# Kernel tuning notes

Measured on AMD Instinct MI355X. Metric: run time of the kernel, lower is better.

## Reference

```python
import jax, jax.numpy as jnp
import numpy as np

N_ATOMS = 200000
N_EDGES = 6400000
N_TYPES = 4
COULOMB = 14.399645478425668  # e^2 / (4 pi eps0) in eV*Angstrom
P_EXP = 0.23
A0 = 0.4685


def _phi(r, c, da):
    # r: (E,), c: (4,), da: (4, E) -> (E,)
    return jnp.sum(c[:, None] * jnp.exp(-r * da), axis=0)


def _dphi(r, c, da):
    return jnp.sum(-c[:, None] * da * jnp.exp(-r * da), axis=0)


def _d2phi(r, c, da):
    return jnp.sum(c[:, None] * da ** 2 * jnp.exp(-r * da), axis=0)


def setup_inputs() -> dict:
    key = jax.random.key(0)
    k1, k2, k3, k4 = jax.random.split(key, 4)
    rij = jax.random.uniform(k1, (N_EDGES,), dtype=jnp.float32) * 2.0 + 0.1
    first_atom = jax.random.randint(k2, (N_EDGES,), 0, N_ATOMS, dtype=jnp.int32)
    second_atom = jax.random.randint(k3, (N_EDGES,), 0, N_ATOMS, dtype=jnp.int32)
    atom_type_index = jax.random.randint(k4, (N_ATOMS,), 0, N_TYPES, dtype=jnp.int32)
    # ASE covalent radii for H, C, N, O (Angstrom) and atomic numbers
    covalent_radii = jnp.array([0.31, 0.76, 0.71, 0.66], dtype=jnp.float32)
    atomic_numbers = jnp.array([1.0, 6.0, 7.0, 8.0], dtype=jnp.float32)
    return {
        "rij": rij,
        "covalent_radii": covalent_radii,
        "atomic_numbers": atomic_numbers,
        "first_atom": first_atom,
        "second_atom": second_atom,
        "atom_type_index": atom_type_index,
        "n_atoms": N_ATOMS,
    }


def reference(rij, covalent_radii, atomic_numbers, first_atom, second_atom, atom_type_index, n_atoms):
    # ZBL 4-term exponential screening coefficients
    c = jnp.array([0.02817, 0.28022, 0.50986, 0.18175], dtype=rij.dtype)
    d = jnp.array([0.20162, 0.4029, 0.94229, 3.1998], dtype=rij.dtype)

    ti = atom_type_index[first_atom]   # (E,)
    tj = atom_type_index[second_atom]  # (E,)
    zi = atomic_numbers[ti]
    zj = atomic_numbers[tj]
    rc = covalent_radii[ti] + covalent_radii[tj]  # outer cutoff per pair

    a = A0 / (zi ** P_EXP + zj ** P_EXP)  # (E,)
    da = d[:, None] / a                    # (4, E)
    factor = COULOMB * zi * zj             # (E,)

    # energy at rij
    e = factor / rij * _phi(rij, c, da)

    # switching polynomial matched at rc (r1 = 0)
    phi_c = _phi(rc, c, da)
    dphi_c = _dphi(rc, c, da)
    d2phi_c = _d2phi(rc, c, da)
    ec = factor / rc * phi_c
    dec = factor / rc * (-phi_c / rc + dphi_c)
    d2ec = factor / rc * (d2phi_c - 2.0 / rc * dphi_c + 2.0 * phi_c / rc ** 2)

    A = (-3.0 * dec + rc * d2ec) / rc ** 2
    B = (2.0 * dec - rc * d2ec) / rc ** 3
    C = -ec + rc * dec / 2.0 - rc * rc * d2ec / 12.0

    e = e + A / 3.0 * rij ** 3 + B / 4.0 * rij ** 4 + C
    e = e / 2.0
    e = jnp.where(rij > rc, jnp.zeros_like(e), e)

    # scatter pair energies onto first atom of each pair
    e_nodes = jax.ops.segment_sum(e, first_atom, num_segments=n_atoms)
    return e_nodes
```

## Files before the change

kernel.cpp:

```cpp
#include <hip/hip_runtime.h>


#define TPB_PACK  256
#define P1_BLOCKS 512
#define P1_TPB    1024
#define SB_BITS   14
#define SBS       (1 << SB_BITS)
#define NS_FUSE   13
#define NS_MAX    16
#define P2_TPB    1024
#define R_SUB     39
#define TPB_RED   256
#define CAP_MAX   1024

#define TAB_N   258
#define TAB_L0  (-3.3219281f)
#define TAB_HL  (0.017157490f)
#define TAB_INV (58.283567f)
#define TAB_OFF (193.61423f)

__global__ __launch_bounds__(P1_TPB) void zbl_bin3(
    const float* __restrict__ rij,
    const float* __restrict__ rcov,
    const float* __restrict__ znum,
    const int*  __restrict__ fa,
    const int*  __restrict__ sa,
    const int*  __restrict__ types,
    unsigned int* __restrict__ regions,
    int*   __restrict__ counts,
    uint2* __restrict__ ovf,
    int E, int nquad, int natoms, int nwords, int NS, int cap, int chunkQ,
    int ovfStride)
{
    __shared__ unsigned s_pk[NS_FUSE * SBS / 16];
    __shared__ float  tabE[16 * TAB_N];
    __shared__ float4 cB[16];
    __shared__ float4 cS[16];
    __shared__ float  cC[16];
    __shared__ int    scnt[NS_MAX];
    __shared__ int    s_ovfn;

    const int b   = blockIdx.x;
    const int tid = threadIdx.x;

    if (tid < NS)  scnt[tid] = 0;
    if (tid == 32) s_ovfn = 0;

    {
        const int4* t4 = (const int4*)types;
        for (int w = tid; w < nwords; w += P1_TPB) {
            unsigned word = 0;
            if (((w << 4) + 16) <= natoms) {
                int b4 = w << 2;
                #pragma unroll
                for (int g = 0; g < 4; ++g) {
                    int4 v = t4[b4 + g];
                    word |= ((unsigned)v.x & 3u) << (8 * g + 0);
                    word |= ((unsigned)v.y & 3u) << (8 * g + 2);
                    word |= ((unsigned)v.z & 3u) << (8 * g + 4);
                    word |= ((unsigned)v.w & 3u) << (8 * g + 6);
                }
            } else {
                int base = w << 4;
                for (int j = 0; j < 16; ++j) {
                    int i = base + j;
                    unsigned t = (i < natoms) ? (unsigned)types[i] : 0u;
                    word |= (t & 3u) << (2 * j);
                }
            }
            s_pk[w] = word;
        }
    }

    if (tid < 16) {
        const float cc[4] = {0.02817f, 0.28022f, 0.50986f, 0.18175f};
        const float dd[4] = {0.20162f, 0.4029f, 0.94229f, 3.1998f};
        const float COUL = 14.399645478425668f;
        int t = tid;
        int ti = t >> 2, tj = t & 3;
        float zi = znum[ti], zj = znum[tj];
        float rc = rcov[ti] + rcov[tj];
        float a = 0.4685f / (powf(zi, 0.23f) + powf(zj, 0.23f));
        float inva = 1.0f / a;
        float factor = COUL * zi * zj;
        float da[4], ee[4];
        float phi = 0.0f, dphi = 0.0f, d2phi = 0.0f;
        #pragma unroll
        for (int k = 0; k < 4; ++k) {
            da[k] = dd[k] * inva;
            ee[k] = expf(-rc * da[k]);
            phi   += cc[k] * ee[k];
            dphi  -= cc[k] * da[k] * ee[k];
            d2phi += cc[k] * da[k] * da[k] * ee[k];
        }
        float invrc = 1.0f / rc;
        float ec   = factor * invrc * phi;
        float dec  = factor * invrc * (-phi * invrc + dphi);
        float d2ec = factor * invrc * (d2phi - 2.0f * invrc * dphi + 2.0f * phi * invrc * invrc);
        float A = (-3.0f * dec + rc * d2ec) * invrc * invrc;
        float B = (2.0f * dec - rc * d2ec) * invrc * invrc * invrc;
        float Cc = -ec + 0.5f * rc * dec - rc * rc * d2ec * (1.0f / 12.0f);
        const float L2E = 1.4426950408889634f;
        cB[t] = make_float4(rc, 0.5f * factor, A * (1.0f / 6.0f), B * 0.125f);
        cS[t] = make_float4(-da[0] * L2E, -da[1] * L2E, -da[2] * L2E, -da[3] * L2E);
        cC[t] = Cc * 0.5f;
    }
    __syncthreads();

    const float lc0 = -5.1497481f;
    const float lc1 = -1.8353434f;
    const float lc2 = -0.9718340f;
    const float lc3 = -2.4600449f;

    for (int n = tid; n < 16 * TAB_N; n += P1_TPB) {
        int t = n / TAB_N, k = n - t * TAB_N;
        float v = 0.0f;
        if (k <= 256) {
            float r = exp2f(__builtin_fmaf((float)k, TAB_HL, TAB_L0));
            float4 B = cB[t];
            if (r <= B.x) {
                float4 S = cS[t];
                float p = exp2f(__builtin_fmaf(r, S.x, lc0))
                        + exp2f(__builtin_fmaf(r, S.y, lc1))
                        + exp2f(__builtin_fmaf(r, S.z, lc2))
                        + exp2f(__builtin_fmaf(r, S.w, lc3));
                float r3 = r * r * r;
                float poly = __builtin_fmaf(__builtin_fmaf(B.w, r, B.z), r3, cC[t]);
                v = __builtin_fmaf(B.y * p, 1.0f / r, poly);
            }
        }
        tabE[n] = v;
    }
    __syncthreads();

    const float4* rij4 = (const float4*)rij;
    const int4*   fa4  = (const int4*)fa;
    const int4*   sa4  = (const int4*)sa;
    int myreg = b * NS;
    int q0 = b * chunkQ;
    int q1 = q0 + chunkQ; if (q1 > nquad) q1 = nquad;

    for (int q = q0 + tid; q < q1; q += P1_TPB) {
        float4 rv = rij4[q];
        int4   iv = fa4[q];
        int4   jv = sa4[q];
        float ra[4] = {rv.x, rv.y, rv.z, rv.w};
        int   ia[4] = {iv.x, iv.y, iv.z, iv.w};
        int   ja[4] = {jv.x, jv.y, jv.z, jv.w};
        float eo[4];
        #pragma unroll
        for (int k = 0; k < 4; ++k) {
            int i = ia[k], j = ja[k];
            unsigned wi = s_pk[i >> 4], wj = s_pk[j >> 4];
            unsigned ti = (wi >> ((i & 15) * 2)) & 3u;
            unsigned tj = (wj >> ((j & 15) * 2)) & 3u;
            int t = (int)((ti << 2) | tj);
            float kf = __builtin_fmaf(__log2f(ra[k]), TAB_INV, TAB_OFF);
            int ki = (int)kf;
            ki = ki < 0 ? 0 : (ki > 256 ? 256 : ki);
            float frac = kf - (float)ki;
            int base = t * TAB_N + ki;
            float v0 = tabE[base];
            float v1 = tabE[base + 1];
            eo[k] = __builtin_fmaf(v1 - v0, frac, v0);
        }
        #pragma unroll
        for (int k = 0; k < 4; ++k) {
            if (eo[k] != 0.0f) {
                int atom = ia[k];
                int s = atom >> SB_BITS;
                int slot = atomicAdd(&scnt[s], 1);
                if (slot < cap) {
                    unsigned rec = ((__float_as_uint(eo[k]) + 0x2000u) & 0xFFFFC000u)
                                 | (unsigned)(atom & (SBS - 1));
                    regions[(unsigned)((myreg + s) * cap + slot)] = rec;
                } else {
                    int o = atomicAdd(&s_ovfn, 1);
                    ovf[(size_t)b * ovfStride + o] =
                        make_uint2(__float_as_uint(eo[k]), (unsigned)atom);
                }
            }
        }
    }

    if (b == 0) {
        for (int idx = nquad * 4 + tid; idx < E; idx += P1_TPB) {
            int i = fa[idx], j = sa[idx];
            unsigned wi = s_pk[i >> 4], wj = s_pk[j >> 4];
            int t = (int)((((wi >> ((i & 15) * 2)) & 3u) << 2) |
                           ((wj >> ((j & 15) * 2)) & 3u));
            float r = rij[idx];
            float kf = __builtin_fmaf(__log2f(r), TAB_INV, TAB_OFF);
            int ki = (int)kf;
            ki = ki < 0 ? 0 : (ki > 256 ? 256 : ki);
            float frac = kf - (float)ki;
            int base = t * TAB_N + ki;
            float e = __builtin_fmaf(tabE[base + 1] - tabE[base], frac, tabE[base]);
            if (e != 0.0f) {
                int o = atomicAdd(&s_ovfn, 1);
                ovf[(size_t)b * ovfStride + o] =
                    make_uint2(__float_as_uint(e), (unsigned)i);
            }
        }
    }

    __syncthreads();
    if (tid < NS)  counts[tid * P1_BLOCKS + b] = min(scnt[tid], cap);
    if (tid == NS) counts[NS  * P1_BLOCKS + b] = s_ovfn;
}

__global__ __launch_bounds__(P2_TPB) void zbl_agg(
    const unsigned int* __restrict__ regions,
    const int*  __restrict__ counts,
    float* __restrict__ partials,
    int NS, int cap)
{
    __shared__ float acc[SBS];
    int s = blockIdx.x, r = blockIdx.y;
    float4* acc4 = (float4*)acc;
    for (int i = threadIdx.x; i < SBS / 4; i += P2_TPB)
        acc4[i] = make_float4(0.f, 0.f, 0.f, 0.f);
    __syncthreads();
    int wave = threadIdx.x >> 6, lane = threadIdx.x & 63;
    const int NW = P2_TPB >> 6;
    for (int p = r + wave * R_SUB; p < P1_BLOCKS; p += NW * R_SUB) {
        int n = counts[s * P1_BLOCKS + p];
        size_t base = ((size_t)p * NS + s) * (size_t)cap;
        for (int t = lane; t < n; t += 64) {
            unsigned rec = regions[base + t];
            atomicAdd(&acc[rec & (SBS - 1)],
                      __uint_as_float(rec & 0xFFFFC000u));
        }
    }
    __syncthreads();
    float4* dst4 = (float4*)(partials + ((size_t)s * R_SUB + r) * SBS);
    for (int i = threadIdx.x; i < SBS / 4; i += P2_TPB)
        dst4[i] = acc4[i];
}

__global__ __launch_bounds__(TPB_RED) void zbl_red3(
    const float* __restrict__ partials,
    const int*   __restrict__ counts,
    const uint2* __restrict__ ovf,
    float* __restrict__ out,
    int natoms, int NS, int ovfStride)
{
    __shared__ int s_any;
    int tid = threadIdx.x;
    int q = blockIdx.x * TPB_RED + tid;
    int nq = natoms >> 2;

    float4 acc = make_float4(0.f, 0.f, 0.f, 0.f);
    int atom0 = q << 2;
    if (q < nq) {
        int s = atom0 >> SB_BITS, i = atom0 & (SBS - 1);
        const float* p = partials + (size_t)s * R_SUB * SBS + i;
        #pragma unroll
        for (int k = 0; k < R_SUB; ++k) {
            float4 v = *(const float4*)(p + (size_t)k * SBS);
            acc.x += v.x; acc.y += v.y; acc.z += v.z; acc.w += v.w;
        }
    }

    if (tid == 0) s_any = 0;
    __syncthreads();
    for (int p0 = tid; p0 < P1_BLOCKS; p0 += TPB_RED) {
        int n = counts[NS * P1_BLOCKS + p0];
        if (n > 0) atomicAdd(&s_any, n);
    }
    __syncthreads();
    if (s_any > 0 && q < nq) {
        for (int p = 0; p < P1_BLOCKS; ++p) {
            int n = counts[NS * P1_BLOCKS + p];
            const uint2* lst = ovf + (size_t)p * ovfStride;
            for (int e = 0; e < n; ++e) {
                uint2 rec = lst[e];
                int d = (int)rec.y - atom0;
                if ((unsigned)d < 4u) {
                    float v = __uint_as_float(rec.x);
                    if      (d == 0) acc.x += v;
                    else if (d == 1) acc.y += v;
                    else if (d == 2) acc.z += v;
                    else             acc.w += v;
                }
            }
        }
    }
    if (q < nq) *(float4*)(out + atom0) = acc;

    if (blockIdx.x == 0 && tid < (natoms & 3)) {
        int atom = (nq << 2) + tid;
        int s = atom >> SB_BITS, i = atom & (SBS - 1);
        const float* p = partials + (size_t)s * R_SUB * SBS + i;
        float a = 0.f;
        #pragma unroll
        for (int k = 0; k < R_SUB; ++k) a += p[(size_t)k * SBS];
        if (s_any > 0) {
            for (int pp = 0; pp < P1_BLOCKS; ++pp) {
                int n = counts[NS * P1_BLOCKS + pp];
                const uint2* lst = ovf + (size_t)pp * ovfStride;
                for (int e = 0; e < n; ++e)
                    if ((int)lst[e].y == atom) a += __uint_as_float(lst[e].x);
            }
        }
        out[atom] = a;
    }
}

__global__ __launch_bounds__(TPB_PACK) void zbl_pack(
    const int* __restrict__ types, unsigned int* __restrict__ packed,
    float* __restrict__ fallback, int natoms, int nwords)
{
    int tid = blockIdx.x * TPB_PACK + threadIdx.x;
    int nth = gridDim.x * TPB_PACK;
    for (int w = tid; w < nwords; w += nth) {
        int base = w << 4;
        unsigned int word = 0;
        #pragma unroll
        for (int j = 0; j < 16; ++j) {
            int i = base + j;
            unsigned int t = (i < natoms) ? (unsigned int)types[i] : 0u;
            word |= (t & 3u) << (2 * j);
        }
        packed[w] = word;
    }
    for (int i = tid; i < natoms; i += nth) fallback[i] = 0.0f;
}

__global__ __launch_bounds__(P1_TPB) void zbl_bin(
    const float* __restrict__ rij, const float* __restrict__ rcov,
    const float* __restrict__ znum, const int* __restrict__ fa,
    const int* __restrict__ sa, const unsigned int* __restrict__ packed,
    unsigned int* __restrict__ regions, int* __restrict__ counts,
    float* __restrict__ fallback,
    int E, int nquad, int natoms, int nwords, int NS, int cap, int chunkQ)
{
    extern __shared__ unsigned int s_packed[];
    __shared__ float  tabE[16 * TAB_N];
    __shared__ float4 cB[16];
    __shared__ float4 cS[16];
    __shared__ float  cC[16];
    __shared__ int scnt[NS_MAX];

    for (int w = threadIdx.x; w < nwords; w += P1_TPB) s_packed[w] = packed[w];
    if (threadIdx.x < NS) scnt[threadIdx.x] = 0;

    if (threadIdx.x < 16) {
        const float cc[4] = {0.02817f, 0.28022f, 0.50986f, 0.18175f};
        const float dd[4] = {0.20162f, 0.4029f, 0.94229f, 3.1998f};
        const float COUL = 14.399645478425668f;
        int t = threadIdx.x;
        int ti = t >> 2, tj = t & 3;
        float zi = znum[ti], zj = znum[tj];
        float rc = rcov[ti] + rcov[tj];
        float a = 0.4685f / (powf(zi, 0.23f) + powf(zj, 0.23f));
        float inva = 1.0f / a;
        float factor = COUL * zi * zj;
        float da[4], ee[4];
        float phi = 0.0f, dphi = 0.0f, d2phi = 0.0f;
        #pragma unroll
        for (int k = 0; k < 4; ++k) {
            da[k] = dd[k] * inva;
            ee[k] = expf(-rc * da[k]);
            phi   += cc[k] * ee[k];
            dphi  -= cc[k] * da[k] * ee[k];
            d2phi += cc[k] * da[k] * da[k] * ee[k];
        }
        float invrc = 1.0f / rc;
        float ec   = factor * invrc * phi;
        float dec  = factor * invrc * (-phi * invrc + dphi);
        float d2ec = factor * invrc * (d2phi - 2.0f * invrc * dphi + 2.0f * phi * invrc * invrc);
        float A = (-3.0f * dec + rc * d2ec) * invrc * invrc;
        float B = (2.0f * dec - rc * d2ec) * invrc * invrc * invrc;
        float Cc = -ec + 0.5f * rc * dec - rc * rc * d2ec * (1.0f / 12.0f);
        const float L2E = 1.4426950408889634f;
        cB[t] = make_float4(rc, 0.5f * factor, A * (1.0f / 6.0f), B * 0.125f);
        cS[t] = make_float4(-da[0] * L2E, -da[1] * L2E, -da[2] * L2E, -da[3] * L2E);
        cC[t] = Cc * 0.5f;
    }
    __syncthreads();

    const float lc0 = -5.1497481f, lc1 = -1.8353434f;
    const float lc2 = -0.9718340f, lc3 = -2.4600449f;

    for (int n = threadIdx.x; n < 16 * TAB_N; n += P1_TPB) {
        int t = n / TAB_N, k = n - t * TAB_N;
        float v = 0.0f;
        if (k <= 256) {
            float r = exp2f(__builtin_fmaf((float)k, TAB_HL, TAB_L0));
            float4 B = cB[t];
            if (r <= B.x) {
                float4 S = cS[t];
                float p = exp2f(__builtin_fmaf(r, S.x, lc0))
                        + exp2f(__builtin_fmaf(r, S.y, lc1))
                        + exp2f(__builtin_fmaf(r, S.z, lc2))
                        + exp2f(__builtin_fmaf(r, S.w, lc3));
                float r3 = r * r * r;
                float poly = __builtin_fmaf(__builtin_fmaf(B.w, r, B.z), r3, cC[t]);
                v = __builtin_fmaf(B.y * p, 1.0f / r, poly);
            }
        }
        tabE[n] = v;
    }
    __syncthreads();

    const float4* rij4 = (const float4*)rij;
    const int4*   fa4  = (const int4*)fa;
    const int4*   sa4  = (const int4*)sa;
    int myreg = blockIdx.x * NS;
    int q0 = blockIdx.x * chunkQ;
    int q1 = q0 + chunkQ; if (q1 > nquad) q1 = nquad;

    for (int q = q0 + threadIdx.x; q < q1; q += P1_TPB) {
        float4 rv = rij4[q];
        int4   iv = fa4[q];
        int4   jv = sa4[q];
        float ra[4] = {rv.x, rv.y, rv.z, rv.w};
        int   ia[4] = {iv.x, iv.y, iv.z, iv.w};
        int   ja[4] = {jv.x, jv.y, jv.z, jv.w};
        float eo[4];
        #pragma unroll
        for (int k = 0; k < 4; ++k) {
            int i = ia[k], j = ja[k];
            unsigned int wi = s_packed[i >> 4], wj = s_packed[j >> 4];
            unsigned int ti = (wi >> ((i & 15) * 2)) & 3u;
            unsigned int tj = (wj >> ((j & 15) * 2)) & 3u;
            int t = (int)((ti << 2) | tj);
            float kf = __builtin_fmaf(__log2f(ra[k]), TAB_INV, TAB_OFF);
            int ki = (int)kf;
            ki = ki < 0 ? 0 : (ki > 256 ? 256 : ki);
            float frac = kf - (float)ki;
            int base = t * TAB_N + ki;
            float v0 = tabE[base], v1 = tabE[base + 1];
            eo[k] = __builtin_fmaf(v1 - v0, frac, v0);
        }
        #pragma unroll
        for (int k = 0; k < 4; ++k) {
            if (eo[k] != 0.0f) {
                int atom = ia[k];
                int s = atom >> SB_BITS;
                int slot = atomicAdd(&scnt[s], 1);
                if (slot < cap) {
                    unsigned rec = ((__float_as_uint(eo[k]) + 0x2000u) & 0xFFFFC000u)
                                 | (unsigned)(atom & (SBS - 1));
                    regions[(unsigned)((myreg + s) * cap + slot)] = rec;
                } else {
                    unsafeAtomicAdd(&fallback[atom], eo[k]);
                }
            }
        }
    }

    if (blockIdx.x == 0) {
        for (int idx = nquad * 4 + threadIdx.x; idx < E; idx += P1_TPB) {
            int i = fa[idx], j = sa[idx];
            unsigned int wi = s_packed[i >> 4], wj = s_packed[j >> 4];
            int t = (int)((((wi >> ((i & 15) * 2)) & 3u) << 2) |
                           ((wj >> ((j & 15) * 2)) & 3u));
            float r = rij[idx];
            float kf = __builtin_fmaf(__log2f(r), TAB_INV, TAB_OFF);
            int ki = (int)kf;
            ki = ki < 0 ? 0 : (ki > 256 ? 256 : ki);
            float frac = kf - (float)ki;
            int base = t * TAB_N + ki;
            float e = __builtin_fmaf(tabE[base + 1] - tabE[base], frac, tabE[base]);
            if (e != 0.0f) unsafeAtomicAdd(&fallback[i], e);
        }
    }

    __syncthreads();
    if (cap > 0 && threadIdx.x < NS)
        counts[threadIdx.x * P1_BLOCKS + blockIdx.x] = min(scnt[threadIdx.x], cap);
}

__global__ __launch_bounds__(TPB_RED) void zbl_red(
    const float* __restrict__ partials, const float* __restrict__ fallback,
    float* __restrict__ out, int natoms)
{
    int q = blockIdx.x * TPB_RED + threadIdx.x;
    int nq = natoms >> 2;
    if (q < nq) {
        int atom = q << 2;
        int s = atom >> SB_BITS, i = atom & (SBS - 1);
        const float4* fb4 = (const float4*)(fallback + atom);
        float4 acc = *fb4;
        const float* p = partials + (size_t)s * R_SUB * SBS + i;
        #pragma unroll
        for (int k = 0; k < R_SUB; ++k) {
            float4 v = *(const float4*)(p + (size_t)k * SBS);
            acc.x += v.x; acc.y += v.y; acc.z += v.z; acc.w += v.w;
        }
        *(float4*)(out + atom) = acc;
    }
    if (blockIdx.x == 0 && threadIdx.x < (natoms & 3)) {
        int atom = (nq << 2) + threadIdx.x;
        int s = atom >> SB_BITS, i = atom & (SBS - 1);
        float acc = fallback[atom];
        const float* p = partials + (size_t)s * R_SUB * SBS + i;
        #pragma unroll
        for (int k = 0; k < R_SUB; ++k) acc += p[(size_t)k * SBS];
        out[atom] = acc;
    }
}

static inline size_t al256(size_t x) { return (x + 255) & ~(size_t)255; }

extern "C" void kernel_launch(void* const* d_in, const int* in_sizes, int n_in,
                              void* d_out, int out_size, void* d_ws, size_t ws_size,
                              hipStream_t stream) {
    const float* rij  = (const float*)d_in[0];
    const float* rcov = (const float*)d_in[1];
    const float* znum = (const float*)d_in[2];
    const int*   fa   = (const int*)d_in[3];
    const int*   sa   = (const int*)d_in[4];
    const int*   types= (const int*)d_in[5];
    float* out = (float*)d_out;
    int E = in_sizes[0];
    int natoms = out_size;
    int nquad = E / 4;
    int nwords = (natoms + 15) / 16;
    int NS = (natoms + SBS - 1) >> SB_BITS;
    if (NS > NS_MAX) NS = NS_MAX;
    int chunkQ = (nquad + P1_BLOCKS - 1) / P1_BLOCKS;
    int ovfStride = chunkQ * 4 + 8;

    if (natoms <= NS_FUSE * SBS) {
        size_t cnt_b  = al256((size_t)(NS + 1) * P1_BLOCKS * 4);
        size_t ovf_b  = al256((size_t)P1_BLOCKS * ovfStride * 8);
        size_t part_b = al256((size_t)NS * R_SUB * SBS * 4);
        char* base = (char*)d_ws;
        int*   counts   = (int*)base;                        base += cnt_b;
        uint2* ovf      = (uint2*)base;                      base += ovf_b;
        float* partials = (float*)base;                      base += part_b;
        unsigned int* regions = (unsigned int*)base;

        long long avail = (long long)ws_size - (long long)(cnt_b + ovf_b + part_b);
        int cap = 0;
        if (avail > 0) cap = (int)(avail / ((long long)P1_BLOCKS * NS * 4));
        if (cap > CAP_MAX) cap = CAP_MAX;

        if (cap >= 64) {
            zbl_bin3<<<P1_BLOCKS, P1_TPB, 0, stream>>>(
                rij, rcov, znum, fa, sa, types,
                regions, counts, ovf,
                E, nquad, natoms, nwords, NS, cap, chunkQ, ovfStride);
            dim3 g2(NS, R_SUB);
            zbl_agg<<<g2, P2_TPB, 0, stream>>>(regions, counts, partials, NS, cap);
            int nq = natoms >> 2;
            zbl_red3<<<(nq + TPB_RED - 1) / TPB_RED, TPB_RED, 0, stream>>>(
                partials, counts, ovf, out, natoms, NS, ovfStride);
            return;
        }
    }

    size_t packed_bytes = al256((size_t)nwords * 4);
    size_t cnt_bytes    = al256((size_t)NS * P1_BLOCKS * 4);
    size_t fb_bytes     = al256((size_t)natoms * 4);
    size_t part_bytes   = al256((size_t)NS * R_SUB * SBS * 4);
    unsigned int* packed = (unsigned int*)d_ws;
    int*   counts   = (int*)  ((char*)d_ws + packed_bytes);
    float* fallback = (float*)((char*)d_ws + packed_bytes + cnt_bytes);
    float* partials = (float*)((char*)d_ws + packed_bytes + cnt_bytes + fb_bytes);
    unsigned int* regions = (unsigned int*)((char*)d_ws + packed_bytes + cnt_bytes
                                            + fb_bytes + part_bytes);
    long long avail = (long long)ws_size
                    - (long long)(packed_bytes + cnt_bytes + fb_bytes + part_bytes);
    int cap = 0;
    if (avail > 0) cap = (int)(avail / ((long long)P1_BLOCKS * (long long)NS * 4));
    if (cap > CAP_MAX) cap = CAP_MAX;
    size_t smem = (size_t)nwords * sizeof(unsigned int);

    if (cap >= 64) {
        zbl_pack<<<96, TPB_PACK, 0, stream>>>(types, packed, fallback, natoms, nwords);
        zbl_bin<<<P1_BLOCKS, P1_TPB, smem, stream>>>(
            rij, rcov, znum, fa, sa, packed, regions, counts, fallback,
            E, nquad, natoms, nwords, NS, cap, chunkQ);
        dim3 g2(NS, R_SUB);
        zbl_agg<<<g2, P2_TPB, 0, stream>>>(regions, counts, partials, NS, cap);
        int nq = natoms >> 2;
        zbl_red<<<(nq + TPB_RED - 1) / TPB_RED, TPB_RED, 0, stream>>>(
            partials, fallback, out, natoms);
    } else {
        zbl_pack<<<96, TPB_PACK, 0, stream>>>(types, packed, out, natoms, nwords);
        zbl_bin<<<P1_BLOCKS, P1_TPB, smem, stream>>>(
            rij, rcov, znum, fa, sa, packed, regions, counts, out,
            E, nquad, natoms, nwords, NS, 0, chunkQ);
    }
}
```

Before: 175.0 us.

## Fuse bin, aggregate and reduce stages into one cooperative kernel

```diff
diff --git a/kernel.cpp b/kernel.cpp
--- a/kernel.cpp
+++ b/kernel.cpp
@@ -1,5 +1,8 @@
 #include <hip/hip_runtime.h>
-
+#include <hip/hip_cooperative_groups.h>
+
+
+namespace cg = cooperative_groups;
 
 #define TPB_PACK  256
 #define P1_BLOCKS 512
@@ -19,58 +22,65 @@
 #define TAB_INV (58.283567f)
 #define TAB_OFF (193.61423f)
 
-__global__ __launch_bounds__(P1_TPB) void zbl_bin3(
+__global__ __launch_bounds__(P1_TPB, 8) void zbl_coop(
     const float* __restrict__ rij,
     const float* __restrict__ rcov,
     const float* __restrict__ znum,
     const int*  __restrict__ fa,
     const int*  __restrict__ sa,
     const int*  __restrict__ types,
+    unsigned int* __restrict__ packed,
     unsigned int* __restrict__ regions,
     int*   __restrict__ counts,
     uint2* __restrict__ ovf,
+    float* __restrict__ partials,
+    float* __restrict__ out,
     int E, int nquad, int natoms, int nwords, int NS, int cap, int chunkQ,
     int ovfStride)
 {
-    __shared__ unsigned s_pk[NS_FUSE * SBS / 16];
-    __shared__ float  tabE[16 * TAB_N];
+    cg::grid_group grid = cg::this_grid();
+
+    __shared__ union {
+        struct { unsigned pk[NS_FUSE * SBS / 16]; float tabE[16 * TAB_N]; } a;
+        float  acc[SBS];
+        float4 acc4[SBS / 4];
+    } u;
     __shared__ float4 cB[16];
     __shared__ float4 cS[16];
     __shared__ float  cC[16];
     __shared__ int    scnt[NS_MAX];
     __shared__ int    s_ovfn;
+    __shared__ int    s_any;
 
     const int b   = blockIdx.x;
     const int tid = threadIdx.x;
 
+    for (int w = b + P1_BLOCKS * tid; w < nwords; w += P1_BLOCKS * P1_TPB) {
+        unsigned word = 0;
+        if (((w << 4) + 16) <= natoms) {
+            const int4* t4 = (const int4*)types;
+            int b4 = w << 2;
+            #pragma unroll
+            for (int g = 0; g < 4; ++g) {
+                int4 v = t4[b4 + g];
+                word |= ((unsigned)v.x & 3u) << (8 * g + 0);
+                word |= ((unsigned)v.y & 3u) << (8 * g + 2);
+                word |= ((unsigned)v.z & 3u) << (8 * g + 4);
+                word |= ((unsigned)v.w & 3u) << (8 * g + 6);
+            }
+        } else {
+            int base = w << 4;
+            for (int j = 0; j < 16; ++j) {
+                int i = base + j;
+                unsigned t = (i < natoms) ? (unsigned)types[i] : 0u;
+                word |= (t & 3u) << (2 * j);
+            }
+        }
+        packed[w] = word;
+    }
+
     if (tid < NS)  scnt[tid] = 0;
     if (tid == 32) s_ovfn = 0;
-
-    {
-        const int4* t4 = (const int4*)types;
-        for (int w = tid; w < nwords; w += P1_TPB) {
-            unsigned word = 0;
-            if (((w << 4) + 16) <= natoms) {
-                int b4 = w << 2;
-                #pragma unroll
-                for (int g = 0; g < 4; ++g) {
-                    int4 v = t4[b4 + g];
-                    word |= ((unsigned)v.x & 3u) << (8 * g + 0);
-                    word |= ((unsigned)v.y & 3u) << (8 * g + 2);
-                    word |= ((unsigned)v.z & 3u) << (8 * g + 4);
-                    word |= ((unsigned)v.w & 3u) << (8 * g + 6);
-                }
-            } else {
-                int base = w << 4;
-                for (int j = 0; j < 16; ++j) {
-                    int i = base + j;
-                    unsigned t = (i < natoms) ? (unsigned)types[i] : 0u;
-                    word |= (t & 3u) << (2 * j);
-                }
-            }
-            s_pk[w] = word;
-        }
-    }
 
     if (tid < 16) {
         const float cc[4] = {0.02817f, 0.28022f, 0.50986f, 0.18175f};
@@ -107,203 +117,209 @@
     }
     __syncthreads();
 
-    const float lc0 = -5.1497481f;
-    const float lc1 = -1.8353434f;
-    const float lc2 = -0.9718340f;
-    const float lc3 = -2.4600449f;
-
-    for (int n = tid; n < 16 * TAB_N; n += P1_TPB) {
-        int t = n / TAB_N, k = n - t * TAB_N;
-        float v = 0.0f;
-        if (k <= 256) {
-            float r = exp2f(__builtin_fmaf((float)k, TAB_HL, TAB_L0));
-            float4 B = cB[t];
-            if (r <= B.x) {
-                float4 S = cS[t];
-                float p = exp2f(__builtin_fmaf(r, S.x, lc0))
-                        + exp2f(__builtin_fmaf(r, S.y, lc1))
-                        + exp2f(__builtin_fmaf(r, S.z, lc2))
-                        + exp2f(__builtin_fmaf(r, S.w, lc3));
-                float r3 = r * r * r;
-                float poly = __builtin_fmaf(__builtin_fmaf(B.w, r, B.z), r3, cC[t]);
-                v = __builtin_fmaf(B.y * p, 1.0f / r, poly);
-            }
-        }
-        tabE[n] = v;
-    }
-    __syncthreads();
-
-    const float4* rij4 = (const float4*)rij;
-    const int4*   fa4  = (const int4*)fa;
-    const int4*   sa4  = (const int4*)sa;
-    int myreg = b * NS;
-    int q0 = b * chunkQ;
-    int q1 = q0 + chunkQ; if (q1 > nquad) q1 = nquad;
-
-    for (int q = q0 + tid; q < q1; q += P1_TPB) {
-        float4 rv = rij4[q];
-        int4   iv = fa4[q];
-        int4   jv = sa4[q];
-        float ra[4] = {rv.x, rv.y, rv.z, rv.w};
-        int   ia[4] = {iv.x, iv.y, iv.z, iv.w};
-        int   ja[4] = {jv.x, jv.y, jv.z, jv.w};
-        float eo[4];
-        #pragma unroll
-        for (int k = 0; k < 4; ++k) {
-            int i = ia[k], j = ja[k];
-            unsigned wi = s_pk[i >> 4], wj = s_pk[j >> 4];
-            unsigned ti = (wi >> ((i & 15) * 2)) & 3u;
-            unsigned tj = (wj >> ((j & 15) * 2)) & 3u;
-            int t = (int)((ti << 2) | tj);
-            float kf = __builtin_fmaf(__log2f(ra[k]), TAB_INV, TAB_OFF);
-            int ki = (int)kf;
-            ki = ki < 0 ? 0 : (ki > 256 ? 256 : ki);
-            float frac = kf - (float)ki;
-            int base = t * TAB_N + ki;
-            float v0 = tabE[base];
-            float v1 = tabE[base + 1];
-            eo[k] = __builtin_fmaf(v1 - v0, frac, v0);
-        }
-        #pragma unroll
-        for (int k = 0; k < 4; ++k) {
-            if (eo[k] != 0.0f) {
-                int atom = ia[k];
-                int s = atom >> SB_BITS;
-                int slot = atomicAdd(&scnt[s], 1);
-                if (slot < cap) {
-                    unsigned rec = ((__float_as_uint(eo[k]) + 0x2000u) & 0xFFFFC000u)
-                                 | (unsigned)(atom & (SBS - 1));
-                    regions[(unsigned)((myreg + s) * cap + slot)] = rec;
-                } else {
+    {
+        const float lc0 = -5.1497481f;
+        const float lc1 = -1.8353434f;
+        const float lc2 = -0.9718340f;
+        const float lc3 = -2.4600449f;
+        for (int n = tid; n < 16 * TAB_N; n += P1_TPB) {
+            int t = n / TAB_N, k = n - t * TAB_N;
+            float v = 0.0f;
+            if (k <= 256) {
+                float r = exp2f(__builtin_fmaf((float)k, TAB_HL, TAB_L0));
+                float4 B = cB[t];
+                if (r <= B.x) {
+                    float4 S = cS[t];
+                    float p = exp2f(__builtin_fmaf(r, S.x, lc0))
+                            + exp2f(__builtin_fmaf(r, S.y, lc1))
+                            + exp2f(__builtin_fmaf(r, S.z, lc2))
+                            + exp2f(__builtin_fmaf(r, S.w, lc3));
+                    float r3 = r * r * r;
+                    float poly = __builtin_fmaf(__builtin_fmaf(B.w, r, B.z), r3, cC[t]);
+                    v = __builtin_fmaf(B.y * p, 1.0f / r, poly);
+                }
+            }
+            u.a.tabE[n] = v;
+        }
+    }
+
+    grid.sync();
+
+    {
+        for (int w = tid; w < nwords; w += P1_TPB)
+            u.a.pk[w] = packed[w];
+        __syncthreads();
+
+        const float4* rij4 = (const float4*)rij;
+        const int4*   fa4  = (const int4*)fa;
+        const int4*   sa4  = (const int4*)sa;
+        int myreg = b * NS;
+        int q0 = b * chunkQ;
+        int q1 = q0 + chunkQ; if (q1 > nquad) q1 = nquad;
+
+        for (int q = q0 + tid; q < q1; q += P1_TPB) {
+            float4 rv = rij4[q];
+            int4   iv = fa4[q];
+            int4   jv = sa4[q];
+            float ra[4] = {rv.x, rv.y, rv.z, rv.w};
+            int   ia[4] = {iv.x, iv.y, iv.z, iv.w};
+            int   ja[4] = {jv.x, jv.y, jv.z, jv.w};
+            float eo[4];
+            #pragma unroll
+            for (int k = 0; k < 4; ++k) {
+                int i = ia[k], j = ja[k];
+                unsigned wi = u.a.pk[i >> 4], wj = u.a.pk[j >> 4];
+                unsigned ti = (wi >> ((i & 15) * 2)) & 3u;
+                unsigned tj = (wj >> ((j & 15) * 2)) & 3u;
+                int t = (int)((ti << 2) | tj);
+                float kf = __builtin_fmaf(__log2f(ra[k]), TAB_INV, TAB_OFF);
+                int ki = (int)kf;
+                ki = ki < 0 ? 0 : (ki > 256 ? 256 : ki);
+                float frac = kf - (float)ki;
+                int base = t * TAB_N + ki;
+                float v0 = u.a.tabE[base];
+                float v1 = u.a.tabE[base + 1];
+                eo[k] = __builtin_fmaf(v1 - v0, frac, v0);
+            }
+            #pragma unroll
+            for (int k = 0; k < 4; ++k) {
+                if (eo[k] != 0.0f) {
+                    int atom = ia[k];
+                    int s = atom >> SB_BITS;
+                    int slot = atomicAdd(&scnt[s], 1);
+                    if (slot < cap) {
+                        unsigned rec = ((__float_as_uint(eo[k]) + 0x2000u) & 0xFFFFC000u)
+                                     | (unsigned)(atom & (SBS - 1));
+                        regions[(unsigned)((myreg + s) * cap + slot)] = rec;
+                    } else {
+                        int o = atomicAdd(&s_ovfn, 1);
+                        ovf[(size_t)b * ovfStride + o] =
+                            make_uint2(__float_as_uint(eo[k]), (unsigned)atom);
+                    }
+                }
+            }
+        }
+
+        if (b == 0) {
+            for (int idx = nquad * 4 + tid; idx < E; idx += P1_TPB) {
+                int i = fa[idx], j = sa[idx];
+                unsigned wi = u.a.pk[i >> 4], wj = u.a.pk[j >> 4];
+                int t = (int)((((wi >> ((i & 15) * 2)) & 3u) << 2) |
+                               ((wj >> ((j & 15) * 2)) & 3u));
+                float r = rij[idx];
+                float kf = __builtin_fmaf(__log2f(r), TAB_INV, TAB_OFF);
+                int ki = (int)kf;
+                ki = ki < 0 ? 0 : (ki > 256 ? 256 : ki);
+                float frac = kf - (float)ki;
+                int base = t * TAB_N + ki;
+                float e = __builtin_fmaf(u.a.tabE[base + 1] - u.a.tabE[base], frac,
+                                         u.a.tabE[base]);
+                if (e != 0.0f) {
                     int o = atomicAdd(&s_ovfn, 1);
                     ovf[(size_t)b * ovfStride + o] =
-                        make_uint2(__float_as_uint(eo[k]), (unsigned)atom);
+                        make_uint2(__float_as_uint(e), (unsigned)i);
                 }
             }
         }
-    }
-
-    if (b == 0) {
-        for (int idx = nquad * 4 + tid; idx < E; idx += P1_TPB) {
-            int i = fa[idx], j = sa[idx];
-            unsigned wi = s_pk[i >> 4], wj = s_pk[j >> 4];
-            int t = (int)((((wi >> ((i & 15) * 2)) & 3u) << 2) |
-                           ((wj >> ((j & 15) * 2)) & 3u));
-            float r = rij[idx];
-            float kf = __builtin_fmaf(__log2f(r), TAB_INV, TAB_OFF);
-            int ki = (int)kf;
-            ki = ki < 0 ? 0 : (ki > 256 ? 256 : ki);
-            float frac = kf - (float)ki;
-            int base = t * TAB_N + ki;
-            float e = __builtin_fmaf(tabE[base + 1] - tabE[base], frac, tabE[base]);
-            if (e != 0.0f) {
-                int o = atomicAdd(&s_ovfn, 1);
-                ovf[(size_t)b * ovfStride + o] =
-                    make_uint2(__float_as_uint(e), (unsigned)i);
-            }
-        }
-    }
-
-    __syncthreads();
-    if (tid < NS)  counts[tid * P1_BLOCKS + b] = min(scnt[tid], cap);
-    if (tid == NS) counts[NS  * P1_BLOCKS + b] = s_ovfn;
-}
-
-__global__ __launch_bounds__(P2_TPB) void zbl_agg(
-    const unsigned int* __restrict__ regions,
-    const int*  __restrict__ counts,
-    float* __restrict__ partials,
-    int NS, int cap)
-{
-    __shared__ float acc[SBS];
-    int s = blockIdx.x, r = blockIdx.y;
-    float4* acc4 = (float4*)acc;
-    for (int i = threadIdx.x; i < SBS / 4; i += P2_TPB)
-        acc4[i] = make_float4(0.f, 0.f, 0.f, 0.f);
-    __syncthreads();
-    int wave = threadIdx.x >> 6, lane = threadIdx.x & 63;
-    const int NW = P2_TPB >> 6;
-    for (int p = r + wave * R_SUB; p < P1_BLOCKS; p += NW * R_SUB) {
-        int n = counts[s * P1_BLOCKS + p];
-        size_t base = ((size_t)p * NS + s) * (size_t)cap;
-        for (int t = lane; t < n; t += 64) {
-            unsigned rec = regions[base + t];
-            atomicAdd(&acc[rec & (SBS - 1)],
-                      __uint_as_float(rec & 0xFFFFC000u));
-        }
-    }
-    __syncthreads();
-    float4* dst4 = (float4*)(partials + ((size_t)s * R_SUB + r) * SBS);
-    for (int i = threadIdx.x; i < SBS / 4; i += P2_TPB)
-        dst4[i] = acc4[i];
-}
-
-__global__ __launch_bounds__(TPB_RED) void zbl_red3(
-    const float* __restrict__ partials,
-    const int*   __restrict__ counts,
-    const uint2* __restrict__ ovf,
-    float* __restrict__ out,
-    int natoms, int NS, int ovfStride)
-{
-    __shared__ int s_any;
-    int tid = threadIdx.x;
-    int q = blockIdx.x * TPB_RED + tid;
-    int nq = natoms >> 2;
-
-    float4 acc = make_float4(0.f, 0.f, 0.f, 0.f);
-    int atom0 = q << 2;
-    if (q < nq) {
-        int s = atom0 >> SB_BITS, i = atom0 & (SBS - 1);
-        const float* p = partials + (size_t)s * R_SUB * SBS + i;
-        #pragma unroll
-        for (int k = 0; k < R_SUB; ++k) {
-            float4 v = *(const float4*)(p + (size_t)k * SBS);
-            acc.x += v.x; acc.y += v.y; acc.z += v.z; acc.w += v.w;
-        }
-    }
-
-    if (tid == 0) s_any = 0;
-    __syncthreads();
-    for (int p0 = tid; p0 < P1_BLOCKS; p0 += TPB_RED) {
-        int n = counts[NS * P1_BLOCKS + p0];
-        if (n > 0) atomicAdd(&s_any, n);
-    }
-    __syncthreads();
-    if (s_any > 0 && q < nq) {
-        for (int p = 0; p < P1_BLOCKS; ++p) {
-            int n = counts[NS * P1_BLOCKS + p];
-            const uint2* lst = ovf + (size_t)p * ovfStride;
-            for (int e = 0; e < n; ++e) {
-                uint2 rec = lst[e];
-                int d = (int)rec.y - atom0;
-                if ((unsigned)d < 4u) {
-                    float v = __uint_as_float(rec.x);
-                    if      (d == 0) acc.x += v;
-                    else if (d == 1) acc.y += v;
-                    else if (d == 2) acc.z += v;
-                    else             acc.w += v;
+
+        __syncthreads();
+        if (tid < NS)  counts[tid * P1_BLOCKS + b] = min(scnt[tid], cap);
+        if (tid == NS) counts[NS  * P1_BLOCKS + b] = s_ovfn;
+    }
+
+    grid.sync();
+
+    if (b < NS * R_SUB) {
+        int s = b / R_SUB, r = b % R_SUB;
+        for (int i = tid; i < SBS / 4; i += P1_TPB)
+            u.acc4[i] = make_float4(0.f, 0.f, 0.f, 0.f);
+        __syncthreads();
+
+        int wave = tid >> 6;
+        int lane = tid & 63;
+        const int NW = P1_TPB >> 6;
+        for (int p = r + wave * R_SUB; p < P1_BLOCKS; p += NW * R_SUB) {
+            int n = counts[s * P1_BLOCKS + p];
+            size_t base = ((size_t)p * NS + s) * (size_t)cap;
+            for (int t = lane; t < n; t += 64) {
+                unsigned rec = regions[base + t];
+                atomicAdd(&u.acc[rec & (SBS - 1)],
+                          __uint_as_float(rec & 0xFFFFC000u));
+            }
+        }
+        __syncthreads();
+
+        float4* dst4 = (float4*)(partials + ((size_t)s * R_SUB + r) * SBS);
+        for (int i = tid; i < SBS / 4; i += P1_TPB)
+            dst4[i] = u.acc4[i];
+    }
+
+    grid.sync();
+
+    {
+        int nq  = natoms >> 2;
+        int qpb = (nq + P1_BLOCKS - 1) / P1_BLOCKS;
+        int qlo = b * qpb, qhi = qlo + qpb;
+        if (qlo > nq) qlo = nq;
+        if (qhi > nq) qhi = nq;
+        bool own_tail = (b == P1_BLOCKS - 1);
+
+        if (tid == 0) s_any = 0;
+        __syncthreads();
+        for (int p0 = tid; p0 < P1_BLOCKS; p0 += P1_TPB) {
+            int n = counts[NS * P1_BLOCKS + p0];
+            if (n > 0) atomicAdd(&s_any, n);
+        }
+        __syncthreads();
+
+        for (int q = qlo + tid; q < qhi; q += P1_TPB) {
+            int atom0 = q << 2;
+            int s = atom0 >> SB_BITS, i = atom0 & (SBS - 1);
+            const float* p = partials + (size_t)s * R_SUB * SBS + i;
+            float4 acc = make_float4(0.f, 0.f, 0.f, 0.f);
+            #pragma unroll
+            for (int k = 0; k < R_SUB; ++k) {
+                float4 v = *(const float4*)(p + (size_t)k * SBS);
+                acc.x += v.x; acc.y += v.y; acc.z += v.z; acc.w += v.w;
+            }
+            if (s_any > 0) {
+                for (int pp = 0; pp < P1_BLOCKS; ++pp) {
+                    int n = counts[NS * P1_BLOCKS + pp];
+                    const uint2* lst = ovf + (size_t)pp * ovfStride;
+                    for (int e = 0; e < n; ++e) {
+                        uint2 rec = lst[e];
+                        int d = (int)rec.y - atom0;
+                        if ((unsigned)d < 4u) {
+                            float v = __uint_as_float(rec.x);
+                            if      (d == 0) acc.x += v;
+                            else if (d == 1) acc.y += v;
+                            else if (d == 2) acc.z += v;
+                            else             acc.w += v;
+                        }
+                    }
                 }
             }
-        }
-    }
-    if (q < nq) *(float4*)(out + atom0) = acc;
-
-    if (blockIdx.x == 0 && tid < (natoms & 3)) {
-        int atom = (nq << 2) + tid;
-        int s = atom >> SB_BITS, i = atom & (SBS - 1);
-        const float* p = partials + (size_t)s * R_SUB * SBS + i;
-        float a = 0.f;
-        #pragma unroll
-        for (int k = 0; k < R_SUB; ++k) a += p[(size_t)k * SBS];
-        if (s_any > 0) {
-            for (int pp = 0; pp < P1_BLOCKS; ++pp) {
-                int n = counts[NS * P1_BLOCKS + pp];
-                const uint2* lst = ovf + (size_t)pp * ovfStride;
-                for (int e = 0; e < n; ++e)
-                    if ((int)lst[e].y == atom) a += __uint_as_float(lst[e].x);
-            }
-        }
-        out[atom] = a;
+            *(float4*)(out + atom0) = acc;
+        }
+
+        if (own_tail) {
+            for (int atom = (nq << 2) + tid; atom < natoms; atom += P1_TPB) {
+                int s = atom >> SB_BITS, i = atom & (SBS - 1);
+                const float* p = partials + (size_t)s * R_SUB * SBS + i;
+                float a = 0.f;
+                #pragma unroll
+                for (int k = 0; k < R_SUB; ++k) a += p[(size_t)k * SBS];
+                if (s_any > 0) {
+                    for (int pp = 0; pp < P1_BLOCKS; ++pp) {
+                        int n = counts[NS * P1_BLOCKS + pp];
+                        const uint2* lst = ovf + (size_t)pp * ovfStride;
+                        for (int e = 0; e < n; ++e)
+                            if ((int)lst[e].y == atom) a += __uint_as_float(lst[e].x);
+                    }
+                }
+                out[atom] = a;
+            }
+        }
     }
 }
 
@@ -473,6 +489,32 @@
         counts[threadIdx.x * P1_BLOCKS + blockIdx.x] = min(scnt[threadIdx.x], cap);
 }
 
+__global__ __launch_bounds__(P2_TPB) void zbl_agg(
+    const unsigned int* __restrict__ regions, const int* __restrict__ counts,
+    float* __restrict__ partials, int NS, int cap)
+{
+    __shared__ float acc[SBS];
+    int s = blockIdx.x, r = blockIdx.y;
+    float4* acc4 = (float4*)acc;
+    for (int i = threadIdx.x; i < SBS / 4; i += P2_TPB)
+        acc4[i] = make_float4(0.f, 0.f, 0.f, 0.f);
+    __syncthreads();
+    int wave = threadIdx.x >> 6, lane = threadIdx.x & 63;
+    const int NW = P2_TPB >> 6;
+    for (int p = r + wave * R_SUB; p < P1_BLOCKS; p += NW * R_SUB) {
+        int n = counts[s * P1_BLOCKS + p];
+        size_t base = ((size_t)p * NS + s) * (size_t)cap;
+        for (int t = lane; t < n; t += 64) {
+            unsigned rec = regions[base + t];
+            atomicAdd(&acc[rec & (SBS - 1)], __uint_as_float(rec & 0xFFFFC000u));
+        }
+    }
+    __syncthreads();
+    float4* dst4 = (float4*)(partials + ((size_t)s * R_SUB + r) * SBS);
+    for (int i = threadIdx.x; i < SBS / 4; i += P2_TPB)
+        dst4[i] = acc4[i];
+}
+
 __global__ __launch_bounds__(TPB_RED) void zbl_red(
     const float* __restrict__ partials, const float* __restrict__ fallback,
     float* __restrict__ out, int natoms)
@@ -504,6 +546,47 @@
 }
 
 static inline size_t al256(size_t x) { return (x + 255) & ~(size_t)255; }
+
+static void launch_legacy(const float* rij, const float* rcov, const float* znum,
+                          const int* fa, const int* sa, const int* types,
+                          float* out, void* d_ws, size_t ws_size,
+                          int E, int nquad, int natoms, int nwords, int NS,
+                          int chunkQ, hipStream_t stream)
+{
+    size_t packed_bytes = al256((size_t)nwords * 4);
+    size_t cnt_bytes    = al256((size_t)NS * P1_BLOCKS * 4);
+    size_t fb_bytes     = al256((size_t)natoms * 4);
+    size_t part_bytes   = al256((size_t)NS * R_SUB * SBS * 4);
+    unsigned int* packed = (unsigned int*)d_ws;
+    int*   counts   = (int*)  ((char*)d_ws + packed_bytes);
+    float* fallback = (float*)((char*)d_ws + packed_bytes + cnt_bytes);
+    float* partials = (float*)((char*)d_ws + packed_bytes + cnt_bytes + fb_bytes);
+    unsigned int* regions = (unsigned int*)((char*)d_ws + packed_bytes + cnt_bytes
+                                            + fb_bytes + part_bytes);
+    long long avail = (long long)ws_size
+                    - (long long)(packed_bytes + cnt_bytes + fb_bytes + part_bytes);
+    int cap = 0;
+    if (avail > 0) cap = (int)(avail / ((long long)P1_BLOCKS * (long long)NS * 4));
+    if (cap > CAP_MAX) cap = CAP_MAX;
+    size_t smem = (size_t)nwords * sizeof(unsigned int);
+
+    if (cap >= 64) {
+        zbl_pack<<<96, TPB_PACK, 0, stream>>>(types, packed, fallback, natoms, nwords);
+        zbl_bin<<<P1_BLOCKS, P1_TPB, smem, stream>>>(
+            rij, rcov, znum, fa, sa, packed, regions, counts, fallback,
+            E, nquad, natoms, nwords, NS, cap, chunkQ);
+        dim3 g2(NS, R_SUB);
+        zbl_agg<<<g2, P2_TPB, 0, stream>>>(regions, counts, partials, NS, cap);
+        int nq = natoms >> 2;
+        zbl_red<<<(nq + TPB_RED - 1) / TPB_RED, TPB_RED, 0, stream>>>(
+            partials, fallback, out, natoms);
+    } else {
+        zbl_pack<<<96, TPB_PACK, 0, stream>>>(types, packed, out, natoms, nwords);
+        zbl_bin<<<P1_BLOCKS, P1_TPB, smem, stream>>>(
+            rij, rcov, znum, fa, sa, packed, regions, counts, out,
+            E, nquad, natoms, nwords, NS, 0, chunkQ);
+    }
+}
 
 extern "C" void kernel_launch(void* const* d_in, const int* in_sizes, int n_in,
                               void* d_out, int out_size, void* d_ws, size_t ws_size,
@@ -525,65 +608,39 @@
     int ovfStride = chunkQ * 4 + 8;
 
     if (natoms <= NS_FUSE * SBS) {
-        size_t cnt_b  = al256((size_t)(NS + 1) * P1_BLOCKS * 4);
-        size_t ovf_b  = al256((size_t)P1_BLOCKS * ovfStride * 8);
-        size_t part_b = al256((size_t)NS * R_SUB * SBS * 4);
+        size_t packed_b = al256((size_t)nwords * 4);
+        size_t cnt_b    = al256((size_t)(NS + 1) * P1_BLOCKS * 4);
+        size_t ovf_b    = al256((size_t)P1_BLOCKS * ovfStride * 8);
+        size_t part_b   = al256((size_t)NS * R_SUB * SBS * 4);
         char* base = (char*)d_ws;
+        unsigned int* packed = (unsigned int*)base;          base += packed_b;
         int*   counts   = (int*)base;                        base += cnt_b;
         uint2* ovf      = (uint2*)base;                      base += ovf_b;
         float* partials = (float*)base;                      base += part_b;
         unsigned int* regions = (unsigned int*)base;
 
-        long long avail = (long long)ws_size - (long long)(cnt_b + ovf_b + part_b);
+        long long avail = (long long)ws_size
+                        - (long long)(packed_b + cnt_b + ovf_b + part_b);
         int cap = 0;
         if (avail > 0) cap = (int)(avail / ((long long)P1_BLOCKS * NS * 4));
         if (cap > CAP_MAX) cap = CAP_MAX;
 
         if (cap >= 64) {
-            zbl_bin3<<<P1_BLOCKS, P1_TPB, 0, stream>>>(
-                rij, rcov, znum, fa, sa, types,
-                regions, counts, ovf,
-                E, nquad, natoms, nwords, NS, cap, chunkQ, ovfStride);
-            dim3 g2(NS, R_SUB);
-            zbl_agg<<<g2, P2_TPB, 0, stream>>>(regions, counts, partials, NS, cap);
-            int nq = natoms >> 2;
-            zbl_red3<<<(nq + TPB_RED - 1) / TPB_RED, TPB_RED, 0, stream>>>(
-                partials, counts, ovf, out, natoms, NS, ovfStride);
-            return;
-        }
-    }
-
-    size_t packed_bytes = al256((size_t)nwords * 4);
-    size_t cnt_bytes    = al256((size_t)NS * P1_BLOCKS * 4);
-    size_t fb_bytes     = al256((size_t)natoms * 4);
-    size_t part_bytes   = al256((size_t)NS * R_SUB * SBS * 4);
-    unsigned int* packed = (unsigned int*)d_ws;
-    int*   counts   = (int*)  ((char*)d_ws + packed_bytes);
-    float* fallback = (float*)((char*)d_ws + packed_bytes + cnt_bytes);
-    float* partials = (float*)((char*)d_ws + packed_bytes + cnt_bytes + fb_bytes);
-    unsigned int* regions = (unsigned int*)((char*)d_ws + packed_bytes + cnt_bytes
-                                            + fb_bytes + part_bytes);
-    long long avail = (long long)ws_size
-                    - (long long)(packed_bytes + cnt_bytes + fb_bytes + part_bytes);
-    int cap = 0;
-    if (avail > 0) cap = (int)(avail / ((long long)P1_BLOCKS * (long long)NS * 4));
-    if (cap > CAP_MAX) cap = CAP_MAX;
-    size_t smem = (size_t)nwords * sizeof(unsigned int);
-
-    if (cap >= 64) {
-        zbl_pack<<<96, TPB_PACK, 0, stream>>>(types, packed, fallback, natoms, nwords);
-        zbl_bin<<<P1_BLOCKS, P1_TPB, smem, stream>>>(
-            rij, rcov, znum, fa, sa, packed, regions, counts, fallback,
-            E, nquad, natoms, nwords, NS, cap, chunkQ);
-        dim3 g2(NS, R_SUB);
-        zbl_agg<<<g2, P2_TPB, 0, stream>>>(regions, counts, partials, NS, cap);
-        int nq = natoms >> 2;
-        zbl_red<<<(nq + TPB_RED - 1) / TPB_RED, TPB_RED, 0, stream>>>(
-            partials, fallback, out, natoms);
-    } else {
-        zbl_pack<<<96, TPB_PACK, 0, stream>>>(types, packed, out, natoms, nwords);
-        zbl_bin<<<P1_BLOCKS, P1_TPB, smem, stream>>>(
-            rij, rcov, znum, fa, sa, packed, regions, counts, out,
-            E, nquad, natoms, nwords, NS, 0, chunkQ);
-    }
+            void* args[] = {
+                (void*)&rij, (void*)&rcov, (void*)&znum,
+                (void*)&fa, (void*)&sa, (void*)&types,
+                (void*)&packed, (void*)&regions, (void*)&counts, (void*)&ovf,
+                (void*)&partials, (void*)&out,
+                (void*)&E, (void*)&nquad, (void*)&natoms, (void*)&nwords,
+                (void*)&NS, (void*)&cap, (void*)&chunkQ, (void*)&ovfStride
+            };
+            hipError_t err = hipLaunchCooperativeKernel(
+                (const void*)zbl_coop, dim3(P1_BLOCKS), dim3(P1_TPB),
+                args, 0, stream);
+            if (err == hipSuccess) return;
+        }
+    }
+
+    launch_legacy(rij, rcov, znum, fa, sa, types, out, d_ws, ws_size,
+                  E, nquad, natoms, nwords, NS, chunkQ, stream);
 }
```

After: 327.7 us. +87.2%, slower.
